# Kernel optimization log

Hardware: AMD Instinct MI355X
Metric: run time of the kernel (lower is better)

The kernel has to match this reference:

```python
import jax, jax.numpy as jnp
import numpy as np

B, C, H, W = 4, 256, 64, 64
C8 = C // 8

def setup_inputs() -> dict:
    key = jax.random.key(0)
    ks = jax.random.split(key, 7)
    s = 0.05
    return {
        "x": jax.random.normal(ks[0], (B, C, H, W), dtype=jnp.float32),
        "wq": jax.random.normal(ks[1], (C8, C), dtype=jnp.float32) * s,
        "bq": jax.random.normal(ks[2], (C8,), dtype=jnp.float32) * s,
        "wk": jax.random.normal(ks[3], (C8, C), dtype=jnp.float32) * s,
        "bk": jax.random.normal(ks[4], (C8,), dtype=jnp.float32) * s,
        "wv": jax.random.normal(ks[5], (C, C), dtype=jnp.float32) * s,
        "bv": jax.random.normal(ks[6], (C,), dtype=jnp.float32) * s,
    }

def reference(x, wq, bq, wk, bk, wv, bv):
    b, c, h, w = x.shape
    n = h * w
    xf = x.reshape(b, c, n)                                   # [B,C,N]
    q = jnp.einsum('oc,bcn->bon', wq, xf) + bq[:, None]       # [B,C/8,N]
    k = jnp.einsum('oc,bcn->bon', wk, xf) + bk[:, None]       # [B,C/8,N]
    v = jnp.einsum('oc,bcn->bon', wv, xf) + bv[:, None]       # [B,C,N]
    # attention[b, i, j] = softmax_j( q[b,:,i] . k[b,:,j] )  (no scaling, per original)
    scores = jnp.einsum('bon,bom->bnm', q, k)                 # [B,N,N]
    attn = jax.nn.softmax(scores, axis=-1)
    # out[b,c,i] = sum_j v[b,c,j] * attn[b,i,j]
    out = jnp.einsum('bcm,bnm->bcn', v, attn)                 # [B,C,N]
    return out.reshape(b, c, h, w) + x
```

## Files before the change

### kernel.cpp

```cpp
#include <hip/hip_runtime.h>
#include <cstdint>
#include <cstddef>

#define BB 4
#define CC 256
#define NN 4096
#define CO 32

typedef __attribute__((ext_vector_type(8))) short bf8;
typedef __attribute__((ext_vector_type(4))) float f4;
typedef __attribute__((ext_vector_type(16))) float f16f;
typedef __attribute__((ext_vector_type(2))) unsigned int u32x2;

#define AS1 __attribute__((address_space(1)))
#define AS3 __attribute__((address_space(3)))

__device__ __forceinline__ unsigned short f2bf(float f) {
    union { float f; unsigned int u; } c; c.f = f;
    unsigned int r = c.u + 0x7FFFu + ((c.u >> 16) & 1u);
    return (unsigned short)(r >> 16);
}
__device__ __forceinline__ float bf2f(unsigned short b) {
    union { unsigned int u; float f; } c; c.u = ((unsigned int)b) << 16;
    return c.f;
}
__device__ __forceinline__ unsigned int cvt_pk_bf16(float a, float b) {
    unsigned int r;
    asm("v_cvt_pk_bf16_f32 %0, %1, %2" : "=v"(r) : "v"(a), "v"(b));
    return r;
}

__global__ __launch_bounds__(512, 2) void k_prep(
        const float* __restrict__ x,
        const float* __restrict__ wq, const float* __restrict__ bq,
        const float* __restrict__ wk, const float* __restrict__ bk,
        const float* __restrict__ wv, const float* __restrict__ bv,
        unsigned short* __restrict__ q_hi, unsigned short* __restrict__ q_lo,
        unsigned short* __restrict__ k_hi, unsigned short* __restrict__ k_lo,
        unsigned short* __restrict__ vws) {
    __shared__ float xT[64 * 256];
    int blk = blockIdx.x;
    int it = blk & 63, b = blk >> 6;
    int i0 = it * 64;
    int tid = threadIdx.x, w = tid >> 6, lane = tid & 63;
    int lr = lane & 15, lg = lane >> 4;

    {
        const float* xp = x + (size_t)b * CC * NN + i0;
        int cl = tid >> 4;
        int il = (tid & 15) * 4;
#pragma unroll
        for (int pass = 0; pass < 8; ++pass) {
            int c = pass * 32 + cl;
            f4 v = *(const f4*)(xp + (size_t)c * NN + il);
#pragma unroll
            for (int jj = 0; jj < 4; ++jj) {
                int i = il + jj;
                xT[i * 256 + (((c >> 2) ^ (i & 7)) << 2) + (c & 3)] = v[jj];
            }
        }
    }
    __syncthreads();

    if (w < 4) {
        f4 acc[4] = {};
        for (int ks = 0; ks < 8; ++ks) {
            int i = w * 16 + lr;
            int kc = ks * 32 + lg * 8;
            f4 xa = *(const f4*)&xT[i * 256 + (((kc >> 2) ^ (i & 7)) << 2)];
            f4 xb = *(const f4*)&xT[i * 256 + ((((kc >> 2) + 1) ^ (i & 7)) << 2)];
            bf8 ahi, alo;
#pragma unroll
            for (int e = 0; e < 8; ++e) {
                float f = (e < 4) ? xa[e] : xb[e - 4];
                unsigned short hh = f2bf(f);
                ahi[e] = (short)hh;
                alo[e] = (short)f2bf(f - bf2f(hh));
            }
#pragma unroll
            for (int u = 0; u < 4; ++u) {
                int o = u * 16 + lr;
                const float* wrow = (u < 2) ? (wq + (size_t)o * CC)
                                            : (wk + (size_t)(o - 32) * CC);
                bf8 bhi, blo;
#pragma unroll
                for (int e = 0; e < 8; ++e) {
                    float wvv = wrow[ks * 32 + lg * 8 + e];
                    unsigned short hh = f2bf(wvv);
                    bhi[e] = (short)hh;
                    blo[e] = (short)f2bf(wvv - bf2f(hh));
                }
                acc[u] = __builtin_amdgcn_mfma_f32_16x16x32_bf16(alo, bhi, acc[u], 0, 0, 0);
                acc[u] = __builtin_amdgcn_mfma_f32_16x16x32_bf16(ahi, blo, acc[u], 0, 0, 0);
                acc[u] = __builtin_amdgcn_mfma_f32_16x16x32_bf16(ahi, bhi, acc[u], 0, 0, 0);
            }
        }
#pragma unroll
        for (int u = 0; u < 4; ++u) {
            int o = u * 16 + lr;
            float bias = (u < 2) ? bq[o] : bk[o - 32];
#pragma unroll
            for (int r = 0; r < 4; ++r) {
                int i = i0 + w * 16 + lg * 4 + r;
                float v = acc[u][r] + bias;
                unsigned short hh = f2bf(v);
                unsigned short ll = f2bf(v - bf2f(hh));
                if (u < 2) {
                    size_t off = ((size_t)b * NN + i) * CO + o;
                    q_hi[off] = hh; q_lo[off] = ll;
                } else {
                    size_t off = ((size_t)b * NN + i) * CO + (o - 32);
                    k_hi[off] = hh; k_lo[off] = ll;
                }
            }
        }
    } else {
        int cb = (w - 4) * 64;
        f4 acc[4][4];
#pragma unroll
        for (int u = 0; u < 4; ++u) {
            f4 bias4;
#pragma unroll
            for (int r = 0; r < 4; ++r) bias4[r] = bv[cb + u * 16 + lg * 4 + r];
#pragma unroll
            for (int t = 0; t < 4; ++t) acc[u][t] = bias4;
        }
        for (int ks = 0; ks < 8; ++ks) {
            bf8 bfr[4];
#pragma unroll
            for (int t = 0; t < 4; ++t) {
                int i = t * 16 + lr;
                int kc = ks * 32 + lg * 8;
                f4 xa = *(const f4*)&xT[i * 256 + (((kc >> 2) ^ (i & 7)) << 2)];
                f4 xb = *(const f4*)&xT[i * 256 + ((((kc >> 2) + 1) ^ (i & 7)) << 2)];
#pragma unroll
                for (int e = 0; e < 8; ++e)
                    bfr[t][e] = (short)f2bf((e < 4) ? xa[e] : xb[e - 4]);
            }
#pragma unroll
            for (int u = 0; u < 4; ++u) {
                const float* wrow = wv + (size_t)(cb + u * 16 + lr) * CC + ks * 32 + lg * 8;
                bf8 afr;
#pragma unroll
                for (int e = 0; e < 8; ++e) afr[e] = (short)f2bf(wrow[e]);
#pragma unroll
                for (int t = 0; t < 4; ++t)
                    acc[u][t] = __builtin_amdgcn_mfma_f32_16x16x32_bf16(afr, bfr[t], acc[u][t], 0, 0, 0);
            }
        }
#pragma unroll
        for (int u = 0; u < 4; ++u)
#pragma unroll
            for (int t = 0; t < 4; ++t)
#pragma unroll
                for (int r = 0; r < 4; ++r) {
                    int c = cb + u * 16 + lg * 4 + r;
                    vws[((size_t)b * CC + c) * NN + i0 + t * 16 + lr] = f2bf(acc[u][t][r]);
                }
    }
}

__global__ __launch_bounds__(512, 1) void k_attn(
        const unsigned short* __restrict__ q_hi, const unsigned short* __restrict__ q_lo,
        const unsigned short* __restrict__ k_hi, const unsigned short* __restrict__ k_lo,
        const unsigned short* __restrict__ vws,
        const float* __restrict__ x, float* __restrict__ out) {
    __shared__ __align__(16) unsigned short Vt[2][16384];
    __shared__ __align__(16) unsigned short K2[2][4096];
    __shared__ __align__(16) unsigned short Pt[2][4096];
    __shared__ float lsum_s[2][64];

    int m = blockIdx.x;
    int xcd = m & 7;
    int b = xcd >> 1;
    int qblk = ((m >> 3) << 1) + (xcd & 1);
    int i0 = qblk * 64;
    int tid = threadIdx.x, w = tid >> 6, lane = tid & 63;
    int lr = lane & 15, lg = lane >> 4, lr7 = lr & 7;
    int a = w & 3, h = w >> 2;
    int l31 = lane & 31, hh = lane >> 5;
    int cw = w & 3, qg = w >> 2;

    bf8 qfh, qfl;
    {
        size_t off = ((size_t)b * NN + i0 + a * 16 + lr) * CO + lg * 8;
        qfh = *(const bf8*)(q_hi + off);
        qfl = *(const bf8*)(q_lo + off);
    }

    int l3 = lane >> 3, sl = lane & 7;
    int us = sl ^ l3;
    const unsigned short* kbase = (us < 4) ? (k_hi + (size_t)b * NN * CO + us * 8)
                                           : (k_lo + (size_t)b * NN * CO + (us - 4) * 8);
    const unsigned short* ksrc = kbase + (size_t)(w * 8 + l3) * CO;
    const unsigned short* vsrc = vws + ((size_t)b * CC + w * 32 + l3) * NN + us * 8;

    auto stageK = [&](int jt, int p) {
        int j0 = ((jt < 64) ? jt : 63) * 64;
        __builtin_amdgcn_global_load_lds((const AS1 void*)(ksrc + (size_t)j0 * CO),
            (AS3 void*)(&K2[p][(w * 8) * 64]), 16, 0, 0);
    };
    auto stageV = [&](int jt, int p) {
        int j0 = ((jt < 64) ? jt : 63) * 64;
#pragma unroll
        for (int n = 0; n < 4; ++n) {
            __builtin_amdgcn_global_load_lds((const AS1 void*)(vsrc + (size_t)(n * 8) * NN + j0),
                (AS3 void*)(&Vt[p][(w * 32 + n * 8) * 64]), 16, 0, 0);
        }
    };

    f16f acc0 = {}, acc1 = {};
    float lsum = 0.f;

    auto S_phase = [&](int js) {
        int pk = js & 1;
#pragma unroll
        for (int t = 0; t < 2; ++t) {
            int jl = h * 32 + t * 16 + lr;
            const unsigned short* Kp = &K2[pk][jl * 64];
            bf8 kfh = *(const bf8*)(Kp + ((lg ^ lr7)) * 8);
            bf8 kfl = *(const bf8*)(Kp + (((4 | lg) ^ lr7)) * 8);
            f4 s = {};
            s = __builtin_amdgcn_mfma_f32_16x16x32_bf16(kfh, qfl, s, 0, 0, 0);
            s = __builtin_amdgcn_mfma_f32_16x16x32_bf16(kfl, qfh, s, 0, 0, 0);
            s = __builtin_amdgcn_mfma_f32_16x16x32_bf16(kfh, qfh, s, 0, 0, 0);
            float e0 = __expf(s[0]), e1 = __expf(s[1]), e2 = __expf(s[2]), e3 = __expf(s[3]);
            lsum += (e0 + e1) + (e2 + e3);
            u32x2 d;
            d[0] = cvt_pk_bf16(e0, e1);
            d[1] = cvt_pk_bf16(e2, e3);
            int row = a * 16 + lr;
            int swz = (row ^ (row >> 3)) & 7;
            int slot = (h * 4 + t * 2 + (lg >> 1)) ^ swz;
            *(u32x2*)&Pt[pk][row * 64 + slot * 8 + (lg & 1) * 4] = d;
        }
    };
    auto PV_phase = [&](int jt) {
        int pv = jt & 1;
        int prow = qg * 32 + l31;
        int pswz = (prow ^ (prow >> 3)) & 7;
        const unsigned short* Pr  = &Pt[pv][prow * 64];
        const unsigned short* Vr0 = &Vt[pv][(cw * 64 + l31) * 64];
        const unsigned short* Vr1 = &Vt[pv][(cw * 64 + 32 + l31) * 64];
        int vswz = l31 & 7;
#pragma unroll
        for (int kc = 0; kc < 4; ++kc) {
            bf8 pb = *(const bf8*)(Pr  + (((kc * 2 + hh) ^ pswz)) * 8);
            bf8 v0 = *(const bf8*)(Vr0 + (((kc * 2 + hh) ^ vswz)) * 8);
            bf8 v1 = *(const bf8*)(Vr1 + (((kc * 2 + hh) ^ vswz)) * 8);
            acc0 = __builtin_amdgcn_mfma_f32_32x32x16_bf16(v0, pb, acc0, 0, 0, 0);
            acc1 = __builtin_amdgcn_mfma_f32_32x32x16_bf16(v1, pb, acc1, 0, 0, 0);
        }
    };

    stageK(0, 0);
    stageV(0, 0);
    __builtin_amdgcn_sched_barrier(0);
    asm volatile("s_waitcnt vmcnt(0) lgkmcnt(0)" ::: "memory");
    __builtin_amdgcn_s_barrier();
    __builtin_amdgcn_sched_barrier(0);
    stageK(1, 1);
    S_phase(0);

    for (int jt = 0; jt < 64; ++jt) {
        __builtin_amdgcn_sched_barrier(0);
        asm volatile("s_waitcnt vmcnt(0) lgkmcnt(0)" ::: "memory");
        __builtin_amdgcn_s_barrier();
        __builtin_amdgcn_sched_barrier(0);
        stageV(jt + 1, (jt + 1) & 1);
        stageK(jt + 2, jt & 1);
        if (jt < 63) S_phase(jt + 1);
        __builtin_amdgcn_s_setprio(1);
        PV_phase(jt);
        __builtin_amdgcn_s_setprio(0);
    }

    lsum += __shfl_xor(lsum, 16, 64);
    lsum += __shfl_xor(lsum, 32, 64);
    if (lane < 16) lsum_s[h][a * 16 + lane] = lsum;
    __syncthreads();

    int qloc = qg * 32 + l31;
    float linv = 1.0f / (lsum_s[0][qloc] + lsum_s[1][qloc]);
    int iq = i0 + qloc;
#pragma unroll
    for (int r = 0; r < 16; ++r) {
        int c0 = cw * 64 + (r & 3) + 8 * (r >> 2) + 4 * hh;
        size_t off0 = ((size_t)(b * CC + c0)) * NN + iq;
        out[off0] = acc0[r] * linv + x[off0];
        size_t off1 = ((size_t)(b * CC + c0 + 32)) * NN + iq;
        out[off1] = acc1[r] * linv + x[off1];
    }
}

extern "C" void kernel_launch(void* const* d_in, const int* in_sizes, int n_in,
                              void* d_out, int out_size, void* d_ws, size_t ws_size,
                              hipStream_t stream) {
    const float* x  = (const float*)d_in[0];
    const float* wq = (const float*)d_in[1];
    const float* bq = (const float*)d_in[2];
    const float* wk = (const float*)d_in[3];
    const float* bk = (const float*)d_in[4];
    const float* wv = (const float*)d_in[5];
    const float* bv = (const float*)d_in[6];
    float* out = (float*)d_out;
    char* ws = (char*)d_ws;
    unsigned short* qh = (unsigned short*)(ws);
    unsigned short* ql = (unsigned short*)(ws + 1048576);
    unsigned short* kh = (unsigned short*)(ws + 2097152);
    unsigned short* kl = (unsigned short*)(ws + 3145728);
    unsigned short* vv = (unsigned short*)(ws + 4194304);

    hipLaunchKernelGGL(k_prep, dim3(256), dim3(512), 0, stream,
                       x, wq, bq, wk, bk, wv, bv, qh, ql, kh, kl, vv);
    hipLaunchKernelGGL(k_attn, dim3(256), dim3(512), 0, stream,
                       qh, ql, kh, kl, vv, x, out);
}
```

Before: 110.1 us.

## Split attention blocks over channel halves with warp-specialized score and PV waves

```diff
diff --git a/kernel.cpp b/kernel.cpp
--- a/kernel.cpp
+++ b/kernel.cpp
@@ -29,6 +29,14 @@
     asm("v_cvt_pk_bf16_f32 %0, %1, %2" : "=v"(r) : "v"(a), "v"(b));
     return r;
 }
+
+#define FULL_BARRIER()                                          \
+    do {                                                        \
+        __builtin_amdgcn_sched_barrier(0);                      \
+        asm volatile("s_waitcnt vmcnt(0) lgkmcnt(0)" ::: "memory"); \
+        __builtin_amdgcn_s_barrier();                           \
+        __builtin_amdgcn_sched_barrier(0);                      \
+    } while (0)
 
 __global__ __launch_bounds__(512, 2) void k_prep(
         const float* __restrict__ x,
@@ -160,29 +168,32 @@
     }
 }
 
-__global__ __launch_bounds__(512, 1) void k_attn(
+__global__ __launch_bounds__(512, 4) void k_attn(
         const unsigned short* __restrict__ q_hi, const unsigned short* __restrict__ q_lo,
         const unsigned short* __restrict__ k_hi, const unsigned short* __restrict__ k_lo,
         const unsigned short* __restrict__ vws,
         const float* __restrict__ x, float* __restrict__ out) {
-    __shared__ __align__(16) unsigned short Vt[2][16384];
+    __shared__ __align__(16) unsigned short Vt[2][8192];
     __shared__ __align__(16) unsigned short K2[2][4096];
     __shared__ __align__(16) unsigned short Pt[2][4096];
-    __shared__ float lsum_s[2][64];
+    __shared__ float linv_s[64];
 
     int m = blockIdx.x;
     int xcd = m & 7;
     int b = xcd >> 1;
-    int qblk = ((m >> 3) << 1) + (xcd & 1);
+    int t128 = ((m >> 3) << 1) + (xcd & 1);
+    int qblk = t128 >> 1;
+    int hc = t128 & 1;
     int i0 = qblk * 64;
+    int cb0 = hc * 128;
     int tid = threadIdx.x, w = tid >> 6, lane = tid & 63;
     int lr = lane & 15, lg = lane >> 4, lr7 = lr & 7;
-    int a = w & 3, h = w >> 2;
     int l31 = lane & 31, hh = lane >> 5;
-    int cw = w & 3, qg = w >> 2;
-
-    bf8 qfh, qfl;
-    {
+    int a = w & 3;
+    int cw = w & 3;
+
+    bf8 qfh = {}, qfl = {};
+    if (w < 4) {
         size_t off = ((size_t)b * NN + i0 + a * 16 + lr) * CO + lg * 8;
         qfh = *(const bf8*)(q_hi + off);
         qfl = *(const bf8*)(q_lo + off);
@@ -193,7 +204,7 @@
     const unsigned short* kbase = (us < 4) ? (k_hi + (size_t)b * NN * CO + us * 8)
                                            : (k_lo + (size_t)b * NN * CO + (us - 4) * 8);
     const unsigned short* ksrc = kbase + (size_t)(w * 8 + l3) * CO;
-    const unsigned short* vsrc = vws + ((size_t)b * CC + w * 32 + l3) * NN + us * 8;
+    const unsigned short* vsrc = vws + ((size_t)b * CC + cb0 + w * 16 + l3) * NN + us * 8;
 
     auto stageK = [&](int jt, int p) {
         int j0 = ((jt < 64) ? jt : 63) * 64;
@@ -203,20 +214,22 @@
     auto stageV = [&](int jt, int p) {
         int j0 = ((jt < 64) ? jt : 63) * 64;
 #pragma unroll
-        for (int n = 0; n < 4; ++n) {
+        for (int n = 0; n < 2; ++n) {
             __builtin_amdgcn_global_load_lds((const AS1 void*)(vsrc + (size_t)(n * 8) * NN + j0),
-                (AS3 void*)(&Vt[p][(w * 32 + n * 8) * 64]), 16, 0, 0);
+                (AS3 void*)(&Vt[p][(w * 16 + n * 8) * 64]), 16, 0, 0);
         }
     };
 
-    f16f acc0 = {}, acc1 = {};
+    f16f accA = {}, accB = {};
     float lsum = 0.f;
 
     auto S_phase = [&](int js) {
         int pk = js & 1;
-#pragma unroll
-        for (int t = 0; t < 2; ++t) {
-            int jl = h * 32 + t * 16 + lr;
+        int row = a * 16 + lr;
+        int swz = (row ^ (row >> 3)) & 7;
+#pragma unroll
+        for (int t = 0; t < 4; ++t) {
+            int jl = t * 16 + lr;
             const unsigned short* Kp = &K2[pk][jl * 64];
             bf8 kfh = *(const bf8*)(Kp + ((lg ^ lr7)) * 8);
             bf8 kfl = *(const bf8*)(Kp + (((4 | lg) ^ lr7)) * 8);
@@ -229,67 +242,69 @@
             u32x2 d;
             d[0] = cvt_pk_bf16(e0, e1);
             d[1] = cvt_pk_bf16(e2, e3);
-            int row = a * 16 + lr;
-            int swz = (row ^ (row >> 3)) & 7;
-            int slot = (h * 4 + t * 2 + (lg >> 1)) ^ swz;
+            int slot = (t * 2 + (lg >> 1)) ^ swz;
             *(u32x2*)&Pt[pk][row * 64 + slot * 8 + (lg & 1) * 4] = d;
         }
     };
     auto PV_phase = [&](int jt) {
         int pv = jt & 1;
-        int prow = qg * 32 + l31;
-        int pswz = (prow ^ (prow >> 3)) & 7;
-        const unsigned short* Pr  = &Pt[pv][prow * 64];
-        const unsigned short* Vr0 = &Vt[pv][(cw * 64 + l31) * 64];
-        const unsigned short* Vr1 = &Vt[pv][(cw * 64 + 32 + l31) * 64];
-        int vswz = l31 & 7;
+        int vr = cw * 32 + l31, vsw = vr & 7;
+        const unsigned short* Vr = &Vt[pv][vr * 64];
+        int pr0 = l31,       psw0 = (pr0 ^ (pr0 >> 3)) & 7;
+        int pr1 = 32 + l31,  psw1 = (pr1 ^ (pr1 >> 3)) & 7;
+        const unsigned short* Pr0 = &Pt[pv][pr0 * 64];
+        const unsigned short* Pr1 = &Pt[pv][pr1 * 64];
 #pragma unroll
         for (int kc = 0; kc < 4; ++kc) {
-            bf8 pb = *(const bf8*)(Pr  + (((kc * 2 + hh) ^ pswz)) * 8);
-            bf8 v0 = *(const bf8*)(Vr0 + (((kc * 2 + hh) ^ vswz)) * 8);
-            bf8 v1 = *(const bf8*)(Vr1 + (((kc * 2 + hh) ^ vswz)) * 8);
-            acc0 = __builtin_amdgcn_mfma_f32_32x32x16_bf16(v0, pb, acc0, 0, 0, 0);
-            acc1 = __builtin_amdgcn_mfma_f32_32x32x16_bf16(v1, pb, acc1, 0, 0, 0);
+            int ch = kc * 2 + hh;
+            bf8 vf  = *(const bf8*)(Vr  + ((ch ^ vsw))  * 8);
+            bf8 pb0 = *(const bf8*)(Pr0 + ((ch ^ psw0)) * 8);
+            bf8 pb1 = *(const bf8*)(Pr1 + ((ch ^ psw1)) * 8);
+            accA = __builtin_amdgcn_mfma_f32_32x32x16_bf16(vf, pb0, accA, 0, 0, 0);
+            accB = __builtin_amdgcn_mfma_f32_32x32x16_bf16(vf, pb1, accB, 0, 0, 0);
         }
     };
 
     stageK(0, 0);
     stageV(0, 0);
-    __builtin_amdgcn_sched_barrier(0);
-    asm volatile("s_waitcnt vmcnt(0) lgkmcnt(0)" ::: "memory");
-    __builtin_amdgcn_s_barrier();
-    __builtin_amdgcn_sched_barrier(0);
+    FULL_BARRIER();
     stageK(1, 1);
-    S_phase(0);
+    if (w < 4) S_phase(0);
 
     for (int jt = 0; jt < 64; ++jt) {
-        __builtin_amdgcn_sched_barrier(0);
-        asm volatile("s_waitcnt vmcnt(0) lgkmcnt(0)" ::: "memory");
-        __builtin_amdgcn_s_barrier();
-        __builtin_amdgcn_sched_barrier(0);
+        FULL_BARRIER();
         stageV(jt + 1, (jt + 1) & 1);
         stageK(jt + 2, jt & 1);
-        if (jt < 63) S_phase(jt + 1);
-        __builtin_amdgcn_s_setprio(1);
-        PV_phase(jt);
-        __builtin_amdgcn_s_setprio(0);
-    }
-
-    lsum += __shfl_xor(lsum, 16, 64);
-    lsum += __shfl_xor(lsum, 32, 64);
-    if (lane < 16) lsum_s[h][a * 16 + lane] = lsum;
+        if (w < 4) {
+            if (jt < 63) S_phase(jt + 1);
+        } else {
+            __builtin_amdgcn_s_setprio(1);
+            PV_phase(jt);
+            __builtin_amdgcn_s_setprio(0);
+        }
+    }
+
+    if (w < 4) {
+        lsum += __shfl_xor(lsum, 16, 64);
+        lsum += __shfl_xor(lsum, 32, 64);
+        if (lane < 16) linv_s[a * 16 + lane] = 1.0f / lsum;
+    }
     __syncthreads();
 
-    int qloc = qg * 32 + l31;
-    float linv = 1.0f / (lsum_s[0][qloc] + lsum_s[1][qloc]);
-    int iq = i0 + qloc;
-#pragma unroll
-    for (int r = 0; r < 16; ++r) {
-        int c0 = cw * 64 + (r & 3) + 8 * (r >> 2) + 4 * hh;
-        size_t off0 = ((size_t)(b * CC + c0)) * NN + iq;
-        out[off0] = acc0[r] * linv + x[off0];
-        size_t off1 = ((size_t)(b * CC + c0 + 32)) * NN + iq;
-        out[off1] = acc1[r] * linv + x[off1];
+    if (w >= 4) {
+#pragma unroll
+        for (int qt = 0; qt < 2; ++qt) {
+            const f16f& ac = qt ? accB : accA;
+            int qloc = qt * 32 + l31;
+            float linv = linv_s[qloc];
+            int iq = i0 + qloc;
+#pragma unroll
+            for (int r = 0; r < 16; ++r) {
+                int c = cb0 + cw * 32 + (r & 3) + 8 * (r >> 2) + 4 * hh;
+                size_t off = ((size_t)(b * CC + c)) * NN + iq;
+                out[off] = ac[r] * linv + x[off];
+            }
+        }
     }
 }
 
@@ -313,6 +328,6 @@
 
     hipLaunchKernelGGL(k_prep, dim3(256), dim3(512), 0, stream,
                        x, wq, bq, wk, bk, wv, bv, qh, ql, kh, kl, vv);
-    hipLaunchKernelGGL(k_attn, dim3(256), dim3(512), 0, stream,
+    hipLaunchKernelGGL(k_attn, dim3(512), dim3(512), 0, stream,
                        qh, ql, kh, kl, vv, x, out);
 }
```

Result: faster. 102.5 us (-6.9%).
